# Kernel tuning notes

Measured on AMD Instinct MI355X. Metric: run time of the kernel, lower is better.

## Reference

```python
import jax, jax.numpy as jnp
import numpy as np

B, S = 4, 64
D, H, DFF, L, V = 512, 8, 2048, 2, 32128
DH = D // H
MAX_ITER, PAD_ID, TEMP = 16, 0, 1.0
NEG = -1e9


def rms_norm(x, w):
    # T5-style RMSNorm (no mean subtraction, no bias)
    return x * jax.lax.rsqrt(jnp.mean(x * x, axis=-1, keepdims=True) + 1e-6) * w


def mha(q_in, kv_in, wq, wk, wv, wo, bias):
    b, tq = q_in.shape[:2]
    tk = kv_in.shape[1]
    q = (q_in @ wq).reshape(b, tq, H, DH)
    k = (kv_in @ wk).reshape(b, tk, H, DH)
    v = (kv_in @ wv).reshape(b, tk, H, DH)
    scores = jnp.einsum('bqhd,bkhd->bhqk', q, k) * (1.0 / np.sqrt(DH)) + bias
    attn = jax.nn.softmax(scores, axis=-1)
    out = jnp.einsum('bhqk,bkhd->bqhd', attn, v).reshape(b, tq, D)
    return out @ wo


def setup_inputs() -> dict:
    key = jax.random.key(0)
    ks = iter(jax.random.split(key, 40))
    def w(*shape):
        return jax.random.normal(next(ks), shape, jnp.float32) * 0.02
    return {
        'input_ids': jax.random.randint(next(ks), (B, S), 0, V),
        'attention_mask': jnp.ones((B, S), jnp.float32),
        'emb': w(V, D),
        'enc_wq': w(L, D, D), 'enc_wk': w(L, D, D), 'enc_wv': w(L, D, D), 'enc_wo': w(L, D, D),
        'enc_ln1': jnp.ones((L, D), jnp.float32),
        'enc_w1': w(L, D, DFF), 'enc_w2': w(L, DFF, D),
        'enc_ln2': jnp.ones((L, D), jnp.float32),
        'enc_lnf': jnp.ones((D,), jnp.float32),
        'dec_sq': w(L, D, D), 'dec_sk': w(L, D, D), 'dec_sv': w(L, D, D), 'dec_so': w(L, D, D),
        'dec_ln1': jnp.ones((L, D), jnp.float32),
        'dec_cq': w(L, D, D), 'dec_ck': w(L, D, D), 'dec_cv': w(L, D, D), 'dec_co': w(L, D, D),
        'dec_ln2': jnp.ones((L, D), jnp.float32),
        'dec_w1': w(L, D, DFF), 'dec_w2': w(L, DFF, D),
        'dec_ln3': jnp.ones((L, D), jnp.float32),
        'dec_lnf': jnp.ones((D,), jnp.float32),
        'lm_head': w(D, V),
    }


def _encoder(x, bias, wq, wk, wv, wo, ln1, w1, w2, ln2, lnf):
    for l in range(L):
        h = rms_norm(x, ln1[l])
        x = x + mha(h, h, wq[l], wk[l], wv[l], wo[l], bias)
        h = rms_norm(x, ln2[l])
        x = x + jax.nn.relu(h @ w1[l]) @ w2[l]
    return rms_norm(x, lnf)


def _decoder(y, hs, enc_bias, sq, sk, sv, so, ln1, cq, ck, cv, co, ln2, w1, w2, ln3, lnf):
    t = y.shape[1]
    causal = jnp.where(jnp.tril(jnp.ones((t, t), bool)), 0.0, NEG)[None, None]  # [1,1,t,t]
    x = y
    for l in range(L):
        h = rms_norm(x, ln1[l])
        x = x + mha(h, h, sq[l], sk[l], sv[l], so[l], causal)
        h = rms_norm(x, ln2[l])
        x = x + mha(h, hs, cq[l], ck[l], cv[l], co[l], enc_bias)
        h = rms_norm(x, ln3[l])
        x = x + jax.nn.relu(h @ w1[l]) @ w2[l]
    return rms_norm(x, lnf)


def reference(input_ids, attention_mask, emb, enc_wq, enc_wk, enc_wv, enc_wo, enc_ln1, enc_w1, enc_w2, enc_ln2, enc_lnf, dec_sq, dec_sk, dec_sv, dec_so, dec_ln1, dec_cq, dec_ck, dec_cv, dec_co, dec_ln2, dec_w1, dec_w2, dec_ln3, dec_lnf, lm_head):
    enc_bias = (1.0 - attention_mask)[:, None, None, :] * NEG  # [B,1,1,S]
    hs = _encoder(emb[input_ids], enc_bias, enc_wq, enc_wk, enc_wv, enc_wo, enc_ln1, enc_w1, enc_w2, enc_ln2, enc_lnf)
    n = input_ids.shape[0]
    # decoder starts from the pad-token embedding, like T2A's pad_ids
    y = jnp.broadcast_to(emb[PAD_ID][None, None, :], (n, 1, D))
    probs_h, preds_h = [], []
    for _ in range(MAX_ITER):
        # full decoder re-run on the growing sequence: NO KV cache, as in the source
        dec_out = _decoder(y, hs, enc_bias, dec_sq, dec_sk, dec_sv, dec_so, dec_ln1, dec_cq, dec_ck, dec_cv, dec_co, dec_ln2, dec_w1, dec_w2, dec_ln3, dec_lnf)
        # grammar mask from NextTokens trackers is external state; treated as allow-all (zeros)
        logits = (dec_out[:, -1] @ lm_head) / TEMP  # [B,V]
        probs = jax.nn.softmax(logits, axis=-1)
        probs_h.append(probs)
        preds_h.append(jnp.argmax(probs, axis=-1))
        # differentiable soft embedding lookup: probs @ embedding matrix
        y = jnp.concatenate([y, (probs @ emb)[:, None, :]], axis=1)
    prob_history = jnp.stack(probs_h, axis=1)  # [B,T,V]
    pred_history = jnp.stack(preds_h, axis=1)  # [B,T]
    return prob_history, pred_history == PAD_ID
```

## Files before the change

kernel.cpp:

```cpp
#include <hip/hip_runtime.h>
#include <math.h>

#define BB   4
#define SS   64
#define DD   512
#define HH   8
#define DHH  64
#define DFFF 2048
#define LL   2
#define VV   32128
#define TT   16
#define EPSV 1e-6f
#define NEGB (-1e9f)
#define NTHR 256
#define NCH  502
#define STS  512

#define BSDc ((size_t)131072)
#define DD2c ((size_t)262144)


__global__ __launch_bounds__(NTHR) void k_embed(const int* __restrict__ ids,
        const float* __restrict__ emb, float* __restrict__ xe, float* __restrict__ xd,
        float* __restrict__ accb) {
    int blk = blockIdx.x, tid = threadIdx.x;
    int id = ids[blk];
    const float* src = emb + (size_t)id * DD;
    float* dst = xe + (size_t)blk * DD;
    for (int k = tid; k < DD; k += NTHR) dst[k] = src[k];
    if (blk < BB) {
        float* xdp = xd + (size_t)blk * DD;
        for (int k = tid; k < DD; k += NTHR) xdp[k] = emb[k];
    }
    if (blk == 4) {
        for (int k = tid; k < 2 * LL * 2048; k += NTHR) accb[k] = 0.f;
    }
}

__global__ __launch_bounds__(NTHR) void k_rms(const float* __restrict__ x,
        const float* __restrict__ ln, float* __restrict__ h) {
    __shared__ float sm[NTHR];
    int row = blockIdx.x, tid = threadIdx.x;
    const float* xr = x + (size_t)row * DD;
    float local = 0.f;
    for (int k = tid; k < DD; k += NTHR) { float v = xr[k]; local += v * v; }
    sm[tid] = local; __syncthreads();
    for (int s = 128; s > 0; s >>= 1) { if (tid < s) sm[tid] += sm[tid + s]; __syncthreads(); }
    float scale = 1.0f / sqrtf(sm[0] / DD + EPSV);
    for (int k = tid; k < DD; k += NTHR) h[(size_t)row * DD + k] = xr[k] * scale * ln[k];
}

__device__ __forceinline__ void gemm_part(const float* __restrict__ A,
        const float* __restrict__ W, float* __restrict__ P,
        int K, int N, int tile, int ks, int kcnt, float* sm) {
    float* As0 = sm;
    float* Ws0 = sm + 1040;
    float* As1 = sm + 2064;
    float* Ws1 = sm + 3104;
    const int tid = threadIdx.x, tr = tid >> 4, tc = tid & 15;
    const int nb = N >> 6;
    const int row0 = (tile / nb) * 64, col0 = (tile % nb) * 64;
    const int arow = tid >> 4, acol = tid & 15;
    const int wrow = tid >> 6, wcol = tid & 63;
    const int kb = ks * kcnt * 16;
    float av[4], wv[4];
    {
        int k0 = kb;
        #pragma unroll
        for (int j = 0; j < 4; j++) {
            av[j] = A[(size_t)(row0 + arow + j * 16) * K + k0 + acol];
            wv[j] = W[(size_t)(k0 + wrow + j * 4) * N + col0 + wcol];
        }
        #pragma unroll
        for (int j = 0; j < 4; j++) {
            As0[acol * 65 + arow + j * 16] = av[j];
            Ws0[(wrow + j * 4) * 64 + wcol] = wv[j];
        }
    }
    __syncthreads();
    float acc[4][4] = {};
    for (int s = 0; s < kcnt; s++) {
        float* Ac = (s & 1) ? As1 : As0;
        float* Wc = (s & 1) ? Ws1 : Ws0;
        if (s + 1 < kcnt) {
            int k0 = kb + (s + 1) * 16;
            #pragma unroll
            for (int j = 0; j < 4; j++) {
                av[j] = A[(size_t)(row0 + arow + j * 16) * K + k0 + acol];
                wv[j] = W[(size_t)(k0 + wrow + j * 4) * N + col0 + wcol];
            }
        }
        #pragma unroll
        for (int kk = 0; kk < 16; kk++) {
            float a[4], b[4];
            #pragma unroll
            for (int j = 0; j < 4; j++) { a[j] = Ac[kk * 65 + tr * 4 + j]; b[j] = Wc[kk * 64 + tc * 4 + j]; }
            #pragma unroll
            for (int r = 0; r < 4; r++)
                #pragma unroll
                for (int c = 0; c < 4; c++) acc[r][c] += a[r] * b[c];
        }
        __syncthreads();
        if (s + 1 < kcnt) {
            float* An = (s & 1) ? As0 : As1;
            float* Wn = (s & 1) ? Ws0 : Ws1;
            #pragma unroll
            for (int j = 0; j < 4; j++) {
                An[acol * 65 + arow + j * 16] = av[j];
                Wn[(wrow + j * 4) * 64 + wcol] = wv[j];
            }
            __syncthreads();
        }
    }
    #pragma unroll
    for (int r = 0; r < 4; r++)
        #pragma unroll
        for (int c = 0; c < 4; c++)
            P[(tr * 4 + r) * 64 + tc * 4 + c] = acc[r][c];
}

template<int KS, int KCNT>
__global__ __launch_bounds__(NTHR) void k_sk(const float* __restrict__ A,
        const float* __restrict__ W, float* __restrict__ P, int K, int N) {
    __shared__ float sm[4128];
    int tile = blockIdx.x / KS, ks = blockIdx.x % KS;
    gemm_part(A, W, P + (size_t)blockIdx.x * 4096, K, N, tile, ks, KCNT, sm);
}

template<int KS, int KCNT>
__global__ __launch_bounds__(NTHR) void k_qkvsk(const float* __restrict__ A,
        const float* __restrict__ wq, const float* __restrict__ wk, const float* __restrict__ wv,
        float* __restrict__ P) {
    __shared__ float sm[4128];
    int j = blockIdx.x / KS, ks = blockIdx.x % KS;
    int m = j >> 5, t2 = j & 31;
    const float* W = (m == 0) ? wq : (m == 1 ? wk : wv);
    gemm_part(A, W, P + (size_t)blockIdx.x * 4096, 512, 512, t2, ks, KCNT, sm);
}

template<int KS, int KCNT>
__global__ __launch_bounds__(NTHR) void k_ckcvsk(const float* __restrict__ A,
        const float* __restrict__ wck, const float* __restrict__ wcv, float* __restrict__ P) {
    __shared__ float sm[4128];
    int j = blockIdx.x / KS, ks = blockIdx.x % KS;
    int m = j >> 5, t2 = j & 31;
    const float* W = (m < 2) ? (wck + (size_t)m * DD2c) : (wcv + (size_t)(m - 2) * DD2c);
    gemm_part(A, W, P + (size_t)blockIdx.x * 4096, 512, 512, t2, ks, KCNT, sm);
}

__device__ __forceinline__ void red_part(const float* __restrict__ P, float* __restrict__ C,
        const float* __restrict__ res, int N, int relu, int tile, int sidx, int KS) {
    const int tid = threadIdx.x;
    const int nb = N >> 6;
    const int row0 = (tile / nb) * 64, col0 = (tile % nb) * 64;
    const float* Pb = P + (size_t)sidx * KS * 4096;
    for (int o = tid; o < 4096; o += NTHR) {
        float v = 0.f;
        for (int k = 0; k < KS; k++) v += Pb[(size_t)k * 4096 + o];
        int r = o >> 6, c = o & 63;
        size_t ix = (size_t)(row0 + r) * N + col0 + c;
        if (res) v += res[ix];
        if (relu) v = fmaxf(v, 0.f);
        C[ix] = v;
    }
}

template<int KS>
__global__ __launch_bounds__(NTHR) void k_red(const float* __restrict__ P, float* __restrict__ C,
        const float* __restrict__ res, int N, int relu) {
    red_part(P, C, res, N, relu, blockIdx.x, blockIdx.x, KS);
}

template<int KS>
__global__ __launch_bounds__(NTHR) void k_qkvred(const float* __restrict__ P, float* __restrict__ qkv) {
    int j = blockIdx.x, m = j >> 5, t2 = j & 31;
    red_part(P, qkv + (size_t)m * BSDc, nullptr, 512, 0, t2, j, KS);
}

template<int KS>
__global__ __launch_bounds__(NTHR) void k_ckcvred(const float* __restrict__ P,
        float* __restrict__ cK, float* __restrict__ cV) {
    int j = blockIdx.x, m = j >> 5, t2 = j & 31;
    float* C = (m < 2) ? (cK + (size_t)m * BSDc) : (cV + (size_t)(m - 2) * BSDc);
    red_part(P, C, nullptr, 512, 0, t2, j, KS);
}

__global__ __launch_bounds__(NTHR) void k_eattn(const float* __restrict__ qkv,
        const float* __restrict__ mask, float* __restrict__ o) {
    __shared__ float sm[3 * 64 * 65];
    int job = blockIdx.x;
    int b = job / HH, h = job % HH;
    int tid = threadIdx.x;
    int lane = tid & 63, wave = tid >> 6;
    float* qq = sm;
    float* kk = sm + 64 * 65;
    float* vv = sm + 2 * 64 * 65;
    for (int i = tid; i < SS * DHH; i += NTHR) {
        int s = i >> 6, d = i & 63;
        size_t src = (size_t)(b * SS + s) * DD + h * DHH + d;
        qq[s * 65 + d] = qkv[src];
        kk[s * 65 + d] = qkv[BSDc + src];
        vv[s * 65 + d] = qkv[2 * BSDc + src];
    }
    __syncthreads();
    float bias = (1.0f - mask[b * SS + lane]) * NEGB;
    for (int r = 0; r < 16; r++) {
        int s = wave * 16 + r;
        float sc = 0.f;
        for (int i = 0; i < DHH; i++) sc += qq[s * 65 + i] * kk[lane * 65 + i];
        sc = sc * 0.125f + bias;
        float m = sc;
        for (int o2 = 32; o2 > 0; o2 >>= 1) m = fmaxf(m, __shfl_xor(m, o2));
        float e = expf(sc - m);
        float sum = e;
        for (int o2 = 32; o2 > 0; o2 >>= 1) sum += __shfl_xor(sum, o2);
        float p = e / sum;
        float acc = 0.f;
        for (int t2 = 0; t2 < SS; t2++) acc += __shfl(p, t2) * vv[t2 * 65 + lane];
        o[(size_t)(b * SS + s) * DD + h * DHH + lane] = acc;
    }
}


__device__ __forceinline__ void build_hAT(const float* __restrict__ A, const float* __restrict__ a1,
        const float* __restrict__ a2, const float* __restrict__ ln, float* hAT, float* scl) {
    const int tid = threadIdx.x, lane = tid & 63, wv = tid >> 6;
    for (int k = tid; k < DD; k += NTHR) {
        float4 h;
        h.x = A[k]; h.y = A[DD + k]; h.z = A[2 * DD + k]; h.w = A[3 * DD + k];
        if (a1) { h.x += a1[k]; h.y += a1[DD + k]; h.z += a1[2 * DD + k]; h.w += a1[3 * DD + k]; }
        if (a2) { h.x += a2[k]; h.y += a2[DD + k]; h.z += a2[2 * DD + k]; h.w += a2[3 * DD + k]; }
        *(float4*)(hAT + (size_t)k * 4) = h;
    }
    __syncthreads();
    float loc = 0.f;
    for (int k = lane; k < DD; k += 64) { float x = hAT[k * 4 + wv]; loc += x * x; }
    for (int o = 32; o > 0; o >>= 1) loc += __shfl_xor(loc, o);
    if (lane == 0) scl[wv] = 1.0f / sqrtf(loc / DD + EPSV);
    __syncthreads();
    float s0 = scl[0], s1 = scl[1], s2 = scl[2], s3 = scl[3];
    for (int k = tid; k < DD; k += NTHR) {
        float lw = ln[k];
        float4 h = *(float4*)(hAT + (size_t)k * 4);
        h.x *= s0 * lw; h.y *= s1 * lw; h.z *= s2 * lw; h.w *= s3 * lw;
        *(float4*)(hAT + (size_t)k * 4) = h;
    }
    __syncthreads();
}

template<int K, int NC>
__device__ __forceinline__ void gemv_core(const float* hAT, const float* __restrict__ W,
        int N, int col0, float* red, float* outL) {
    constexpr int C4N = NC / 4;
    constexpr int KSN = NTHR / C4N;
    constexpr int KC  = K / KSN;
    const int tid = threadIdx.x;
    const int c4 = tid % C4N, ks = tid / C4N;
    const float4* W4 = (const float4*)W;
    float acc[4][4] = {};
    const int kb = ks * KC;
    #pragma unroll 8
    for (int kk = 0; kk < KC; kk++) {
        int k = kb + kk;
        float4 w4 = W4[(size_t)k * (N >> 2) + (col0 >> 2) + c4];
        float4 h4 = *(const float4*)(hAT + (size_t)k * 4);
        float hb[4] = {h4.x, h4.y, h4.z, h4.w};
        float wb[4] = {w4.x, w4.y, w4.z, w4.w};
        #pragma unroll
        for (int b = 0; b < 4; b++)
            #pragma unroll
            for (int ci = 0; ci < 4; ci++) acc[b][ci] += hb[b] * wb[ci];
    }
    {
        float* rp = red + (size_t)ks * (NC * 4) + c4 * 4;
        #pragma unroll
        for (int b = 0; b < 4; b++)
            #pragma unroll
            for (int ci = 0; ci < 4; ci++) rp[b * NC + ci] = acc[b][ci];
    }
    __syncthreads();
    for (int o = tid; o < 4 * NC; o += NTHR) {
        float v = 0.f;
        #pragma unroll
        for (int k2 = 0; k2 < KSN; k2++) v += red[(size_t)k2 * (NC * 4) + o];
        outL[o] = v;
    }
    __syncthreads();
}

__device__ __forceinline__ void oproj_add(const float* attT, const float* __restrict__ Wo,
        int h, float* accD, float* red) {
    const int tid = threadIdx.x;
    const int c4 = tid & 127, ks = tid >> 7;
    const float4* W4 = (const float4*)Wo;
    float ac[4][4] = {};
    const int db = ks * 32;
    #pragma unroll 8
    for (int dd = 0; dd < 32; dd++) {
        int d = db + dd;
        float4 w4 = W4[(size_t)(h * DHH + d) * 128 + c4];
        float wb[4] = {w4.x, w4.y, w4.z, w4.w};
        #pragma unroll
        for (int bb = 0; bb < 4; bb++) {
            float av = attT[d * 4 + bb];
            #pragma unroll
            for (int ci = 0; ci < 4; ci++) ac[bb][ci] += av * wb[ci];
        }
    }
    {
        float* rp = red + ks * 2048 + c4 * 4;
        #pragma unroll
        for (int bb = 0; bb < 4; bb++)
            #pragma unroll
            for (int ci = 0; ci < 4; ci++) rp[bb * 512 + ci] = ac[bb][ci];
    }
    __syncthreads();
    for (int o = tid; o < 2048; o += NTHR) {
        atomicAdd(accD + o, red[o] + red[2048 + o]);
    }
}

__global__ __launch_bounds__(NTHR) void k_self(const float* __restrict__ xc,
        const float* __restrict__ ln1, const float* __restrict__ Wq,
        const float* __restrict__ Wk, const float* __restrict__ Wv,
        const float* __restrict__ Wso, float* __restrict__ sKl, float* __restrict__ sVl,
        float* __restrict__ aS, int tt) {
    __shared__ float hAT[2048];
    __shared__ float red[4096];
    __shared__ float scl[4];
    __shared__ float qh[256];
    __shared__ float kh[256];
    __shared__ float vh[256];
    __shared__ float attT[256];
    const int h = blockIdx.x;
    const int tid = threadIdx.x, lane = tid & 63, b = tid >> 6;

    build_hAT(xc, nullptr, nullptr, ln1, hAT, scl);
    gemv_core<512, 64>(hAT, Wq, 512, h * 64, red, qh);
    gemv_core<512, 64>(hAT, Wk, 512, h * 64, red, kh);
    gemv_core<512, 64>(hAT, Wv, 512, h * 64, red, vh);
    {
        int c = tid & 63;
        size_t dst = ((size_t)b * TT + tt) * DD + h * DHH + c;
        sKl[dst] = kh[tid];
        sVl[dst] = vh[tid];
    }
    float sc = -1e30f;
    if (lane <= tt) {
        float s2 = 0.f;
        if (lane == tt) {
            #pragma unroll 16
            for (int i = 0; i < DHH; i++) s2 += qh[b * 64 + i] * kh[b * 64 + i];
        } else {
            const float* kr = sKl + ((size_t)b * TT + lane) * DD + h * DHH;
            #pragma unroll 16
            for (int i = 0; i < DHH; i++) s2 += qh[b * 64 + i] * kr[i];
        }
        sc = s2 * 0.125f;
    }
    float m = sc;
    for (int o2 = 32; o2 > 0; o2 >>= 1) m = fmaxf(m, __shfl_xor(m, o2));
    float e = (lane <= tt) ? expf(sc - m) : 0.f;
    float sum = e;
    for (int o2 = 32; o2 > 0; o2 >>= 1) sum += __shfl_xor(sum, o2);
    float pr = e / sum;
    float acc = 0.f;
    for (int j = 0; j < tt; j++) {
        float pj = __shfl(pr, j);
        acc += pj * sVl[((size_t)b * TT + j) * DD + h * DHH + lane];
    }
    acc += __shfl(pr, tt) * vh[b * 64 + lane];
    attT[lane * 4 + b] = acc;
    __syncthreads();
    oproj_add(attT, Wso, h, aS, red);
}

__global__ __launch_bounds__(NTHR) void k_cross(const float* __restrict__ xc,
        const float* __restrict__ aS, const float* __restrict__ ln2,
        const float* __restrict__ Wcq, const float* __restrict__ Wco,
        const float* __restrict__ cKl, const float* __restrict__ cVl,
        const float* __restrict__ mask, float* __restrict__ aC) {
    __shared__ float hAT[2048];
    __shared__ float red[4096];
    __shared__ float scl[4];
    __shared__ float qh[256];
    __shared__ float prS[256];
    __shared__ float attT[256];
    const int h = blockIdx.x;
    const int tid = threadIdx.x, lane = tid & 63, b = tid >> 6;

    build_hAT(xc, aS, nullptr, ln2, hAT, scl);
    gemv_core<512, 64>(hAT, Wcq, 512, h * 64, red, qh);
    const float* kr = cKl + ((size_t)b * SS + lane) * DD + h * DHH;
    float s2 = 0.f;
    #pragma unroll 16
    for (int i = 0; i < DHH; i++) s2 += qh[b * 64 + i] * kr[i];
    float sc = s2 * 0.125f + (1.0f - mask[b * SS + lane]) * NEGB;
    float m = sc;
    for (int o2 = 32; o2 > 0; o2 >>= 1) m = fmaxf(m, __shfl_xor(m, o2));
    float e = expf(sc - m);
    float sum = e;
    for (int o2 = 32; o2 > 0; o2 >>= 1) sum += __shfl_xor(sum, o2);
    prS[b * 64 + lane] = e / sum;
    const float* vbase = cVl + (size_t)b * SS * DD + h * DHH + lane;
    float a0 = 0.f, a1 = 0.f, a2 = 0.f, a3 = 0.f;
    #pragma unroll 4
    for (int j = 0; j < SS; j += 4) {
        a0 += prS[b * 64 + j]     * vbase[(size_t)j * DD];
        a1 += prS[b * 64 + j + 1] * vbase[(size_t)(j + 1) * DD];
        a2 += prS[b * 64 + j + 2] * vbase[(size_t)(j + 2) * DD];
        a3 += prS[b * 64 + j + 3] * vbase[(size_t)(j + 3) * DD];
    }
    attT[lane * 4 + b] = (a0 + a1) + (a2 + a3);
    __syncthreads();
    oproj_add(attT, Wco, h, aC, red);
}

template<int K, int NC>
__global__ __launch_bounds__(NTHR) void k_gemv(const float* __restrict__ A,
        const float* __restrict__ a1, const float* __restrict__ a2, const float* __restrict__ ln,
        const float* __restrict__ W, float* __restrict__ O, int ostr, int N,
        const float* __restrict__ res, const float* __restrict__ r1, const float* __restrict__ r2,
        int relu) {
    constexpr int C4N = NC / 4;
    constexpr int KSN = NTHR / C4N;
    constexpr int KC  = K / KSN;
    __shared__ float sm[K * 4 + 4096 + 4];
    float* hAT = sm;
    float* red = sm + K * 4;
    float* scl = sm + K * 4 + 4096;
    const int tid = threadIdx.x, lane = tid & 63, wv = tid >> 6;
    for (int k = tid; k < K; k += NTHR) {
        float4 h;
        h.x = A[k]; h.y = A[K + k]; h.z = A[2 * K + k]; h.w = A[3 * K + k];
        if (a1) { h.x += a1[k]; h.y += a1[K + k]; h.z += a1[2 * K + k]; h.w += a1[3 * K + k]; }
        if (a2) { h.x += a2[k]; h.y += a2[K + k]; h.z += a2[2 * K + k]; h.w += a2[3 * K + k]; }
        *(float4*)(hAT + (size_t)k * 4) = h;
    }
    __syncthreads();
    if (ln) {
        float loc = 0.f;
        for (int k = lane; k < K; k += 64) { float x = hAT[k * 4 + wv]; loc += x * x; }
        for (int o = 32; o > 0; o >>= 1) loc += __shfl_xor(loc, o);
        if (lane == 0) scl[wv] = 1.0f / sqrtf(loc / K + EPSV);
        __syncthreads();
        float s0 = scl[0], s1 = scl[1], s2 = scl[2], s3 = scl[3];
        for (int k = tid; k < K; k += NTHR) {
            float lw = ln[k];
            float4 h = *(float4*)(hAT + (size_t)k * 4);
            h.x *= s0 * lw; h.y *= s1 * lw; h.z *= s2 * lw; h.w *= s3 * lw;
            *(float4*)(hAT + (size_t)k * 4) = h;
        }
    }
    __syncthreads();
    const int c4 = tid % C4N, ks = tid / C4N;
    const float4* W4 = (const float4*)W;
    const int col0 = blockIdx.x * NC;
    float acc[4][4] = {};
    const int kb = ks * KC;
    #pragma unroll 8
    for (int kk = 0; kk < KC; kk++) {
        int k = kb + kk;
        float4 w4 = W4[(size_t)k * (N >> 2) + (col0 >> 2) + c4];
        float4 h4 = *(float4*)(hAT + (size_t)k * 4);
        float hb[4] = {h4.x, h4.y, h4.z, h4.w};
        float wb[4] = {w4.x, w4.y, w4.z, w4.w};
        #pragma unroll
        for (int b = 0; b < 4; b++)
            #pragma unroll
            for (int ci = 0; ci < 4; ci++) acc[b][ci] += hb[b] * wb[ci];
    }
    {
        float* rp = red + (size_t)ks * (NC * 4) + c4 * 4;
        #pragma unroll
        for (int b = 0; b < 4; b++)
            #pragma unroll
            for (int ci = 0; ci < 4; ci++) rp[b * NC + ci] = acc[b][ci];
    }
    __syncthreads();
    for (int o = tid; o < 4 * NC; o += NTHR) {
        int b = o / NC, c = o % NC;
        float v = 0.f;
        #pragma unroll
        for (int k2 = 0; k2 < KSN; k2++) v += red[(size_t)k2 * (NC * 4) + o];
        size_t ix = (size_t)b * ostr + col0 + c;
        if (res) v += res[ix];
        if (r1)  v += r1[ix];
        if (r2)  v += r2[ix];
        if (relu) v = fmaxf(v, 0.f);
        O[ix] = v;
    }
}

__global__ __launch_bounds__(NTHR) void k_lmhead(const float* __restrict__ xc, float* __restrict__ xn,
        const float* __restrict__ lnf, const float* __restrict__ Wlm,
        float* __restrict__ lgb, float* __restrict__ stm, float* __restrict__ sts,
        int* __restrict__ stix, float* __restrict__ accb) {
    int blk = blockIdx.x, tid = threadIdx.x, lane = tid & 63, wave = tid >> 6;
    if (blk >= NCH) {
        for (int k = tid; k < BB * DD; k += NTHR) xn[k] = 0.f;
        for (int k = tid; k < 2 * LL * 2048; k += NTHR) accb[k] = 0.f;
        return;
    }
    __shared__ float hAT[2048];
    __shared__ float red[4096];
    __shared__ float msc[4];
    __shared__ float lgl[256];
    for (int k = tid; k < DD; k += NTHR) {
        float4 r;
        r.x = xc[k];          r.y = xc[DD + k];
        r.z = xc[2 * DD + k]; r.w = xc[3 * DD + k];
        *(float4*)(hAT + (size_t)k * 4) = r;
    }
    __syncthreads();
    {
        float loc = 0.f;
        for (int k = lane; k < DD; k += 64) { float x = hAT[k * 4 + wave]; loc += x * x; }
        for (int o = 32; o > 0; o >>= 1) loc += __shfl_xor(loc, o);
        if (lane == 0) msc[wave] = 1.0f / sqrtf(loc / DD + EPSV);
    }
    __syncthreads();
    float s0 = msc[0], s1 = msc[1], s2 = msc[2], s3 = msc[3];
    for (int k = tid; k < DD; k += NTHR) {
        float lw = lnf[k];
        float4 r = *(float4*)(hAT + (size_t)k * 4);
        r.x *= s0 * lw; r.y *= s1 * lw; r.z *= s2 * lw; r.w *= s3 * lw;
        *(float4*)(hAT + (size_t)k * 4) = r;
    }
    __syncthreads();
    {
        int c4 = tid & 15, ks = tid >> 4;
        const float4* W4 = (const float4*)Wlm;
        float acc[4][4] = {};
        int kb = ks * 32;
        #pragma unroll
        for (int kk = 0; kk < 32; kk++) {
            int k = kb + kk;
            float4 w4 = W4[(size_t)k * (VV >> 2) + blk * 16 + c4];
            float4 h4 = *(float4*)(hAT + (size_t)k * 4);
            float hb[4] = {h4.x, h4.y, h4.z, h4.w};
            float wb[4] = {w4.x, w4.y, w4.z, w4.w};
            #pragma unroll
            for (int b = 0; b < 4; b++)
                #pragma unroll
                for (int ci = 0; ci < 4; ci++) acc[b][ci] += hb[b] * wb[ci];
        }
        float* rp = red + ks * 256 + c4 * 4;
        #pragma unroll
        for (int b = 0; b < 4; b++)
            #pragma unroll
            for (int ci = 0; ci < 4; ci++) rp[b * 64 + ci] = acc[b][ci];
    }
    __syncthreads();
    {
        float v = 0.f;
        #pragma unroll
        for (int k2 = 0; k2 < 16; k2++) v += red[k2 * 256 + tid];
        lgl[tid] = v;
        lgb[(size_t)(tid >> 6) * VV + blk * 64 + (tid & 63)] = v;
    }
    __syncthreads();
    {
        int b = wave;
        float v0 = lgl[b * 64 + lane];
        float mx = v0; int ix = lane;
        for (int o = 32; o > 0; o >>= 1) {
            float om = __shfl_xor(mx, o); int oi = __shfl_xor(ix, o);
            if (om > mx || (om == mx && oi < ix)) { mx = om; ix = oi; }
        }
        float s = expf(v0 - mx);
        for (int o = 32; o > 0; o >>= 1) s += __shfl_xor(s, o);
        if (lane == 0) {
            stm[b * STS + blk] = mx;
            sts[b * STS + blk] = s;
            stix[b * STS + blk] = blk * 64 + ix;
        }
    }
}

__global__ __launch_bounds__(NTHR) void k_dmerge(const float* __restrict__ lgb,
        const float* __restrict__ stm, const float* __restrict__ sts, const int* __restrict__ stix,
        const float* __restrict__ emb, float* __restrict__ out, float* __restrict__ xn, int tt) {
    __shared__ float mM[8];
    __shared__ int jS[4];
    __shared__ float pT[256];
    __shared__ float red[4096];
    int blk = blockIdx.x, tid = threadIdx.x, lane = tid & 63, wave = tid >> 6;
    {
        int b = wave;
        float M = -1e30f, S = 0.f; int jb = 0;
        for (int j = lane; j < NCH; j += 64) {
            float mj = stm[b * STS + j], sj = sts[b * STS + j];
            if (mj > M) { S = S * expf(M - mj) + sj; M = mj; jb = j; }
            else        { S += sj * expf(mj - M); }
        }
        for (int o = 32; o > 0; o >>= 1) {
            float Mo = __shfl_xor(M, o), So = __shfl_xor(S, o);
            int jo = __shfl_xor(jb, o);
            if (Mo > M || (Mo == M && jo < jb)) { S = S * expf(M - Mo) + So; M = Mo; jb = jo; }
            else { S += So * expf(Mo - M); }
        }
        if (lane == 0) { mM[b] = M; mM[4 + b] = S; jS[b] = jb; }
    }
    __syncthreads();
    if (blk < NCH) {
        {
            int b = tid >> 6, c = tid & 63;
            float lg = lgb[(size_t)b * VV + blk * 64 + c];
            float p = expf(lg - mM[b]) / mM[4 + b];
            out[((size_t)b * TT + tt) * VV + blk * 64 + c] = p;
            pT[c * 4 + b] = p;
        }
        __syncthreads();
        {
            int c4 = tid & 127, rs = tid >> 7;
            const float4* E4 = (const float4*)emb;
            float4 a0 = {0,0,0,0}, a1 = a0, a2 = a0, a3 = a0;
            int rb = rs * 32;
            #pragma unroll 8
            for (int r = 0; r < 32; r++) {
                int row = rb + r;
                float4 e4 = E4[((size_t)(blk * 64 + row)) * 128 + c4];
                float4 p4 = *(float4*)(pT + row * 4);
                a0.x += p4.x * e4.x; a0.y += p4.x * e4.y; a0.z += p4.x * e4.z; a0.w += p4.x * e4.w;
                a1.x += p4.y * e4.x; a1.y += p4.y * e4.y; a1.z += p4.y * e4.z; a1.w += p4.y * e4.w;
                a2.x += p4.z * e4.x; a2.y += p4.z * e4.y; a2.z += p4.z * e4.z; a2.w += p4.z * e4.w;
                a3.x += p4.w * e4.x; a3.y += p4.w * e4.y; a3.z += p4.w * e4.z; a3.w += p4.w * e4.w;
            }
            float* rp = red + rs * 2048 + c4 * 4;
            rp[0]        = a0.x; rp[1]        = a0.y; rp[2]        = a0.z; rp[3]        = a0.w;
            rp[512 + 0]  = a1.x; rp[512 + 1]  = a1.y; rp[512 + 2]  = a1.z; rp[512 + 3]  = a1.w;
            rp[1024 + 0] = a2.x; rp[1024 + 1] = a2.y; rp[1024 + 2] = a2.z; rp[1024 + 3] = a2.w;
            rp[1536 + 0] = a3.x; rp[1536 + 1] = a3.y; rp[1536 + 2] = a3.z; rp[1536 + 3] = a3.w;
        }
        __syncthreads();
        #pragma unroll
        for (int i = 0; i < 8; i++) {
            int o = tid + i * 256;
            atomicAdd(xn + o, red[o] + red[2048 + o]);
        }
    } else {
        if (tid < 4) {
            int col = stix[tid * STS + jS[tid]];
            out[(size_t)BB * TT * VV + tid * TT + tt] = (col == 0) ? 1.0f : 0.0f;
        }
    }
}

extern "C" void kernel_launch(void* const* d_in, const int* in_sizes, int n_in,
                              void* d_out, int out_size, void* d_ws, size_t ws_size,
                              hipStream_t stream) {
    const int*   ids     = (const int*)  d_in[0];
    const float* mask    = (const float*)d_in[1];
    const float* emb     = (const float*)d_in[2];
    const float* enc_wq  = (const float*)d_in[3];
    const float* enc_wk  = (const float*)d_in[4];
    const float* enc_wv  = (const float*)d_in[5];
    const float* enc_wo  = (const float*)d_in[6];
    const float* enc_ln1 = (const float*)d_in[7];
    const float* enc_w1  = (const float*)d_in[8];
    const float* enc_w2  = (const float*)d_in[9];
    const float* enc_ln2 = (const float*)d_in[10];
    const float* enc_lnf = (const float*)d_in[11];
    const float* dec_sq  = (const float*)d_in[12];
    const float* dec_sk  = (const float*)d_in[13];
    const float* dec_sv  = (const float*)d_in[14];
    const float* dec_so  = (const float*)d_in[15];
    const float* dec_ln1 = (const float*)d_in[16];
    const float* dec_cq  = (const float*)d_in[17];
    const float* dec_ck  = (const float*)d_in[18];
    const float* dec_cv  = (const float*)d_in[19];
    const float* dec_co  = (const float*)d_in[20];
    const float* dec_ln2 = (const float*)d_in[21];
    const float* dec_w1  = (const float*)d_in[22];
    const float* dec_w2  = (const float*)d_in[23];
    const float* dec_ln3 = (const float*)d_in[24];
    const float* dec_lnf = (const float*)d_in[25];
    const float* lm_head = (const float*)d_in[26];
    float* out = (float*)d_out;

    float* ws    = (float*)d_ws;
    float* xe    = ws;
    float* qkv   = xe + BSDc;
    float* hbuf  = qkv + 3 * BSDc;
    float* attb  = hbuf + BSDc;
    float* ffbuf = attb + BSDc;
    float* cK    = ffbuf + (size_t)BB * SS * DFFF;
    float* cV    = cK + LL * BSDc;
    float* sK    = cV + LL * BSDc;
    float* sV    = sK + (size_t)LL * BB * TT * DD;
    float* xdA   = sV + (size_t)LL * BB * TT * DD;
    float* xdB   = xdA + 2048;
    float* accb  = xdB + 2048;
    float* dff   = accb + 8192;
    float* stm   = dff + 8192;
    float* sts   = stm + 4 * STS;
    int*   stix  = (int*)(sts + 4 * STS);
    float* lgb   = (float*)(stix) + 2048;
    float* skb   = lgb + 4 * VV;

    k_embed<<<256, NTHR, 0, stream>>>(ids, emb, xe, xdA, accb);
    for (int l = 0; l < LL; l++) {
        k_rms<<<256, NTHR, 0, stream>>>(xe, enc_ln1 + (size_t)l * DD, hbuf);
        k_qkvsk<4, 8><<<384, NTHR, 0, stream>>>(hbuf, enc_wq + (size_t)l * DD2c,
                enc_wk + (size_t)l * DD2c, enc_wv + (size_t)l * DD2c, skb);
        k_qkvred<4><<<96, NTHR, 0, stream>>>(skb, qkv);
        k_eattn<<<32, NTHR, 0, stream>>>(qkv, mask, attb);
        k_sk<8, 4><<<256, NTHR, 0, stream>>>(attb, enc_wo + (size_t)l * DD2c, skb, 512, 512);
        k_red<8><<<32, NTHR, 0, stream>>>(skb, xe, xe, 512, 0);
        k_rms<<<256, NTHR, 0, stream>>>(xe, enc_ln2 + (size_t)l * DD, hbuf);
        k_sk<4, 8><<<512, NTHR, 0, stream>>>(hbuf, enc_w1 + (size_t)l * DD * DFFF, skb, 512, 2048);
        k_red<4><<<128, NTHR, 0, stream>>>(skb, ffbuf, nullptr, 2048, 1);
        k_sk<16, 8><<<512, NTHR, 0, stream>>>(ffbuf, enc_w2 + (size_t)l * DFFF * DD, skb, 2048, 512);
        k_red<16><<<32, NTHR, 0, stream>>>(skb, xe, xe, 512, 0);
    }
    k_rms<<<256, NTHR, 0, stream>>>(xe, enc_lnf, hbuf);
    k_ckcvsk<4, 8><<<512, NTHR, 0, stream>>>(hbuf, dec_ck, dec_cv, skb);
    k_ckcvred<4><<<128, NTHR, 0, stream>>>(skb, cK, cV);

    for (int tt = 0; tt < TT; tt++) {
        float* xc = (tt & 1) ? xdB : xdA;
        float* xn = (tt & 1) ? xdA : xdB;
        for (int l = 0; l < LL; l++) {
            float* aS = accb + (size_t)l * 2048;
            float* aC = accb + 4096 + (size_t)l * 2048;
            k_self<<<HH, NTHR, 0, stream>>>(xc, dec_ln1 + (size_t)l * DD,
                    dec_sq + (size_t)l * DD2c, dec_sk + (size_t)l * DD2c,
                    dec_sv + (size_t)l * DD2c, dec_so + (size_t)l * DD2c,
                    sK + (size_t)l * BB * TT * DD, sV + (size_t)l * BB * TT * DD, aS, tt);
            k_cross<<<HH, NTHR, 0, stream>>>(xc, aS, dec_ln2 + (size_t)l * DD,
                    dec_cq + (size_t)l * DD2c, dec_co + (size_t)l * DD2c,
                    cK + (size_t)l * BSDc, cV + (size_t)l * BSDc, mask, aC);
            k_gemv<512, 16><<<128, NTHR, 0, stream>>>(xc, aS, aC, dec_ln3 + (size_t)l * DD,
                    dec_w1 + (size_t)l * DD * DFFF, dff, DFFF, DFFF,
                    nullptr, nullptr, nullptr, 1);
            k_gemv<2048, 8><<<64, NTHR, 0, stream>>>(dff, nullptr, nullptr, nullptr,
                    dec_w2 + (size_t)l * DFFF * DD, xc, DD, 512,
                    xc, aS, aC, 0);
        }
        k_lmhead<<<NCH + 1, NTHR, 0, stream>>>(xc, xn, dec_lnf, lm_head, lgb, stm, sts, stix, accb);
        k_dmerge<<<NCH + 1, NTHR, 0, stream>>>(lgb, stm, sts, stix, emb, out, xn, tt);
    }
}
```

Before: 2.533 ms.

## Fuse decoder FFN up/down into one kernel with atomic residual accumulators

```diff
diff --git a/kernel.cpp b/kernel.cpp
--- a/kernel.cpp
+++ b/kernel.cpp
@@ -15,6 +15,7 @@
 #define NTHR 256
 #define NCH  502
 #define STS  512
+#define NACCT (3 * LL)
 
 #define BSDc ((size_t)131072)
 #define DD2c ((size_t)262144)
@@ -33,7 +34,7 @@
         for (int k = tid; k < DD; k += NTHR) xdp[k] = emb[k];
     }
     if (blk == 4) {
-        for (int k = tid; k < 2 * LL * 2048; k += NTHR) accb[k] = 0.f;
+        for (int k = tid; k < NACCT * 2048; k += NTHR) accb[k] = 0.f;
     }
 }
 
@@ -222,14 +223,17 @@
 }
 
 
-__device__ __forceinline__ void build_hAT(const float* __restrict__ A, const float* __restrict__ a1,
-        const float* __restrict__ a2, const float* __restrict__ ln, float* hAT, float* scl) {
+__device__ __forceinline__ void build_hAT_n(const float* __restrict__ x0,
+        const float* __restrict__ accb, int nacc,
+        const float* __restrict__ ln, float* hAT, float* scl) {
     const int tid = threadIdx.x, lane = tid & 63, wv = tid >> 6;
     for (int k = tid; k < DD; k += NTHR) {
         float4 h;
-        h.x = A[k]; h.y = A[DD + k]; h.z = A[2 * DD + k]; h.w = A[3 * DD + k];
-        if (a1) { h.x += a1[k]; h.y += a1[DD + k]; h.z += a1[2 * DD + k]; h.w += a1[3 * DD + k]; }
-        if (a2) { h.x += a2[k]; h.y += a2[DD + k]; h.z += a2[2 * DD + k]; h.w += a2[3 * DD + k]; }
+        h.x = x0[k]; h.y = x0[DD + k]; h.z = x0[2 * DD + k]; h.w = x0[3 * DD + k];
+        for (int a = 0; a < nacc; a++) {
+            const float* ap = accb + (size_t)a * 2048;
+            h.x += ap[k]; h.y += ap[DD + k]; h.z += ap[2 * DD + k]; h.w += ap[3 * DD + k];
+        }
         *(float4*)(hAT + (size_t)k * 4) = h;
     }
     __syncthreads();
@@ -321,10 +325,11 @@
 }
 
 __global__ __launch_bounds__(NTHR) void k_self(const float* __restrict__ xc,
+        const float* __restrict__ accb, float* __restrict__ accw, int nacc,
         const float* __restrict__ ln1, const float* __restrict__ Wq,
         const float* __restrict__ Wk, const float* __restrict__ Wv,
         const float* __restrict__ Wso, float* __restrict__ sKl, float* __restrict__ sVl,
-        float* __restrict__ aS, int tt) {
+        int tt) {
     __shared__ float hAT[2048];
     __shared__ float red[4096];
     __shared__ float scl[4];
@@ -334,8 +339,9 @@
     __shared__ float attT[256];
     const int h = blockIdx.x;
     const int tid = threadIdx.x, lane = tid & 63, b = tid >> 6;
-
-    build_hAT(xc, nullptr, nullptr, ln1, hAT, scl);
+    float* aS = accw + (size_t)nacc * 2048;
+
+    build_hAT_n(xc, accb, nacc, ln1, hAT, scl);
     gemv_core<512, 64>(hAT, Wq, 512, h * 64, red, qh);
     gemv_core<512, 64>(hAT, Wk, 512, h * 64, red, kh);
     gemv_core<512, 64>(hAT, Wv, 512, h * 64, red, vh);
@@ -376,10 +382,10 @@
 }
 
 __global__ __launch_bounds__(NTHR) void k_cross(const float* __restrict__ xc,
-        const float* __restrict__ aS, const float* __restrict__ ln2,
-        const float* __restrict__ Wcq, const float* __restrict__ Wco,
-        const float* __restrict__ cKl, const float* __restrict__ cVl,
-        const float* __restrict__ mask, float* __restrict__ aC) {
+        const float* __restrict__ accb, float* __restrict__ accw, int nacc,
+        const float* __restrict__ ln2, const float* __restrict__ Wcq,
+        const float* __restrict__ Wco, const float* __restrict__ cKl,
+        const float* __restrict__ cVl, const float* __restrict__ mask) {
     __shared__ float hAT[2048];
     __shared__ float red[4096];
     __shared__ float scl[4];
@@ -388,8 +394,9 @@
     __shared__ float attT[256];
     const int h = blockIdx.x;
     const int tid = threadIdx.x, lane = tid & 63, b = tid >> 6;
-
-    build_hAT(xc, aS, nullptr, ln2, hAT, scl);
+    float* aC = accw + (size_t)nacc * 2048;
+
+    build_hAT_n(xc, accb, nacc, ln2, hAT, scl);
     gemv_core<512, 64>(hAT, Wcq, 512, h * 64, red, qh);
     const float* kr = cKl + ((size_t)b * SS + lane) * DD + h * DHH;
     float s2 = 0.f;
@@ -416,118 +423,66 @@
     oproj_add(attT, Wco, h, aC, red);
 }
 
-template<int K, int NC>
-__global__ __launch_bounds__(NTHR) void k_gemv(const float* __restrict__ A,
-        const float* __restrict__ a1, const float* __restrict__ a2, const float* __restrict__ ln,
-        const float* __restrict__ W, float* __restrict__ O, int ostr, int N,
-        const float* __restrict__ res, const float* __restrict__ r1, const float* __restrict__ r2,
-        int relu) {
-    constexpr int C4N = NC / 4;
-    constexpr int KSN = NTHR / C4N;
-    constexpr int KC  = K / KSN;
-    __shared__ float sm[K * 4 + 4096 + 4];
-    float* hAT = sm;
-    float* red = sm + K * 4;
-    float* scl = sm + K * 4 + 4096;
-    const int tid = threadIdx.x, lane = tid & 63, wv = tid >> 6;
-    for (int k = tid; k < K; k += NTHR) {
-        float4 h;
-        h.x = A[k]; h.y = A[K + k]; h.z = A[2 * K + k]; h.w = A[3 * K + k];
-        if (a1) { h.x += a1[k]; h.y += a1[K + k]; h.z += a1[2 * K + k]; h.w += a1[3 * K + k]; }
-        if (a2) { h.x += a2[k]; h.y += a2[K + k]; h.z += a2[2 * K + k]; h.w += a2[3 * K + k]; }
-        *(float4*)(hAT + (size_t)k * 4) = h;
-    }
-    __syncthreads();
-    if (ln) {
-        float loc = 0.f;
-        for (int k = lane; k < K; k += 64) { float x = hAT[k * 4 + wv]; loc += x * x; }
-        for (int o = 32; o > 0; o >>= 1) loc += __shfl_xor(loc, o);
-        if (lane == 0) scl[wv] = 1.0f / sqrtf(loc / K + EPSV);
-        __syncthreads();
-        float s0 = scl[0], s1 = scl[1], s2 = scl[2], s3 = scl[3];
-        for (int k = tid; k < K; k += NTHR) {
-            float lw = ln[k];
-            float4 h = *(float4*)(hAT + (size_t)k * 4);
-            h.x *= s0 * lw; h.y *= s1 * lw; h.z *= s2 * lw; h.w *= s3 * lw;
-            *(float4*)(hAT + (size_t)k * 4) = h;
-        }
-    }
-    __syncthreads();
-    const int c4 = tid % C4N, ks = tid / C4N;
-    const float4* W4 = (const float4*)W;
-    const int col0 = blockIdx.x * NC;
-    float acc[4][4] = {};
-    const int kb = ks * KC;
-    #pragma unroll 8
-    for (int kk = 0; kk < KC; kk++) {
-        int k = kb + kk;
-        float4 w4 = W4[(size_t)k * (N >> 2) + (col0 >> 2) + c4];
-        float4 h4 = *(float4*)(hAT + (size_t)k * 4);
-        float hb[4] = {h4.x, h4.y, h4.z, h4.w};
-        float wb[4] = {w4.x, w4.y, w4.z, w4.w};
-        #pragma unroll
-        for (int b = 0; b < 4; b++)
-            #pragma unroll
-            for (int ci = 0; ci < 4; ci++) acc[b][ci] += hb[b] * wb[ci];
-    }
-    {
-        float* rp = red + (size_t)ks * (NC * 4) + c4 * 4;
-        #pragma unroll
-        for (int b = 0; b < 4; b++)
-            #pragma unroll
-            for (int ci = 0; ci < 4; ci++) rp[b * NC + ci] = acc[b][ci];
-    }
-    __syncthreads();
-    for (int o = tid; o < 4 * NC; o += NTHR) {
-        int b = o / NC, c = o % NC;
-        float v = 0.f;
-        #pragma unroll
-        for (int k2 = 0; k2 < KSN; k2++) v += red[(size_t)k2 * (NC * 4) + o];
-        size_t ix = (size_t)b * ostr + col0 + c;
-        if (res) v += res[ix];
-        if (r1)  v += r1[ix];
-        if (r2)  v += r2[ix];
-        if (relu) v = fmaxf(v, 0.f);
-        O[ix] = v;
+__global__ __launch_bounds__(NTHR) void k_ffn(const float* __restrict__ xc,
+        const float* __restrict__ accb, float* __restrict__ accw, int nacc,
+        const float* __restrict__ ln3, const float* __restrict__ W1,
+        const float* __restrict__ W2) {
+    __shared__ float hAT[2048];
+    __shared__ float red[4096];
+    __shared__ float scl[4];
+    __shared__ float upL[64];
+    const int j = blockIdx.x;
+    const int tid = threadIdx.x;
+    float* aF = accw + (size_t)nacc * 2048;
+
+    build_hAT_n(xc, accb, nacc, ln3, hAT, scl);
+    gemv_core<512, 16>(hAT, W1, DFFF, j * 16, red, upL);
+    {
+        const int c4 = tid & 127, ks = tid >> 7;
+        const float4* W24 = (const float4*)W2;
+        float ac[4][4] = {};
+        const int kb = ks * 8;
+        #pragma unroll
+        for (int kk = 0; kk < 8; kk++) {
+            int row = j * 16 + kb + kk;
+            float4 w4 = W24[(size_t)row * 128 + c4];
+            float wb[4] = {w4.x, w4.y, w4.z, w4.w};
+            #pragma unroll
+            for (int bb = 0; bb < 4; bb++) {
+                float av = fmaxf(upL[bb * 16 + kb + kk], 0.f);
+                #pragma unroll
+                for (int ci = 0; ci < 4; ci++) ac[bb][ci] += av * wb[ci];
+            }
+        }
+        float* rp = red + ks * 2048 + c4 * 4;
+        #pragma unroll
+        for (int bb = 0; bb < 4; bb++)
+            #pragma unroll
+            for (int ci = 0; ci < 4; ci++) rp[bb * 512 + ci] = ac[bb][ci];
+    }
+    __syncthreads();
+    for (int o0 = tid; o0 < 2048; o0 += NTHR) {
+        int bb = o0 >> 9, n = (o0 + j * 16) & 511;
+        int o = bb * 512 + n;
+        atomicAdd(aF + o, red[o] + red[2048 + o]);
     }
 }
 
 __global__ __launch_bounds__(NTHR) void k_lmhead(const float* __restrict__ xc, float* __restrict__ xn,
-        const float* __restrict__ lnf, const float* __restrict__ Wlm,
-        float* __restrict__ lgb, float* __restrict__ stm, float* __restrict__ sts,
-        int* __restrict__ stix, float* __restrict__ accb) {
+        const float* __restrict__ accb, const float* __restrict__ lnf,
+        const float* __restrict__ Wlm, float* __restrict__ lgb, float* __restrict__ stm,
+        float* __restrict__ sts, int* __restrict__ stix, float* __restrict__ accz) {
     int blk = blockIdx.x, tid = threadIdx.x, lane = tid & 63, wave = tid >> 6;
     if (blk >= NCH) {
         for (int k = tid; k < BB * DD; k += NTHR) xn[k] = 0.f;
-        for (int k = tid; k < 2 * LL * 2048; k += NTHR) accb[k] = 0.f;
+        for (int k = tid; k < NACCT * 2048; k += NTHR) accz[k] = 0.f;
         return;
     }
     __shared__ float hAT[2048];
     __shared__ float red[4096];
     __shared__ float msc[4];
     __shared__ float lgl[256];
-    for (int k = tid; k < DD; k += NTHR) {
-        float4 r;
-        r.x = xc[k];          r.y = xc[DD + k];
-        r.z = xc[2 * DD + k]; r.w = xc[3 * DD + k];
-        *(float4*)(hAT + (size_t)k * 4) = r;
-    }
-    __syncthreads();
-    {
-        float loc = 0.f;
-        for (int k = lane; k < DD; k += 64) { float x = hAT[k * 4 + wave]; loc += x * x; }
-        for (int o = 32; o > 0; o >>= 1) loc += __shfl_xor(loc, o);
-        if (lane == 0) msc[wave] = 1.0f / sqrtf(loc / DD + EPSV);
-    }
-    __syncthreads();
-    float s0 = msc[0], s1 = msc[1], s2 = msc[2], s3 = msc[3];
-    for (int k = tid; k < DD; k += NTHR) {
-        float lw = lnf[k];
-        float4 r = *(float4*)(hAT + (size_t)k * 4);
-        r.x *= s0 * lw; r.y *= s1 * lw; r.z *= s2 * lw; r.w *= s3 * lw;
-        *(float4*)(hAT + (size_t)k * 4) = r;
-    }
-    __syncthreads();
+    build_hAT_n(xc, accb, NACCT, lnf, hAT, msc);
     {
         int c4 = tid & 15, ks = tid >> 4;
         const float4* W4 = (const float4*)Wlm;
@@ -692,8 +647,7 @@
     float* xdA   = sV + (size_t)LL * BB * TT * DD;
     float* xdB   = xdA + 2048;
     float* accb  = xdB + 2048;
-    float* dff   = accb + 8192;
-    float* stm   = dff + 8192;
+    float* stm   = accb + NACCT * 2048;
     float* sts   = stm + 4 * STS;
     int*   stix  = (int*)(sts + 4 * STS);
     float* lgb   = (float*)(stix) + 2048;
@@ -722,23 +676,21 @@
         float* xc = (tt & 1) ? xdB : xdA;
         float* xn = (tt & 1) ? xdA : xdB;
         for (int l = 0; l < LL; l++) {
-            float* aS = accb + (size_t)l * 2048;
-            float* aC = accb + 4096 + (size_t)l * 2048;
-            k_self<<<HH, NTHR, 0, stream>>>(xc, dec_ln1 + (size_t)l * DD,
+            k_self<<<HH, NTHR, 0, stream>>>(xc, accb, accb, 3 * l,
+                    dec_ln1 + (size_t)l * DD,
                     dec_sq + (size_t)l * DD2c, dec_sk + (size_t)l * DD2c,
                     dec_sv + (size_t)l * DD2c, dec_so + (size_t)l * DD2c,
-                    sK + (size_t)l * BB * TT * DD, sV + (size_t)l * BB * TT * DD, aS, tt);
-            k_cross<<<HH, NTHR, 0, stream>>>(xc, aS, dec_ln2 + (size_t)l * DD,
+                    sK + (size_t)l * BB * TT * DD, sV + (size_t)l * BB * TT * DD, tt);
+            k_cross<<<HH, NTHR, 0, stream>>>(xc, accb, accb, 3 * l + 1,
+                    dec_ln2 + (size_t)l * DD,
                     dec_cq + (size_t)l * DD2c, dec_co + (size_t)l * DD2c,
-                    cK + (size_t)l * BSDc, cV + (size_t)l * BSDc, mask, aC);
-            k_gemv<512, 16><<<128, NTHR, 0, stream>>>(xc, aS, aC, dec_ln3 + (size_t)l * DD,
-                    dec_w1 + (size_t)l * DD * DFFF, dff, DFFF, DFFF,
-                    nullptr, nullptr, nullptr, 1);
-            k_gemv<2048, 8><<<64, NTHR, 0, stream>>>(dff, nullptr, nullptr, nullptr,
-                    dec_w2 + (size_t)l * DFFF * DD, xc, DD, 512,
-                    xc, aS, aC, 0);
-        }
-        k_lmhead<<<NCH + 1, NTHR, 0, stream>>>(xc, xn, dec_lnf, lm_head, lgb, stm, sts, stix, accb);
+                    cK + (size_t)l * BSDc, cV + (size_t)l * BSDc, mask);
+            k_ffn<<<128, NTHR, 0, stream>>>(xc, accb, accb, 3 * l + 2,
+                    dec_ln3 + (size_t)l * DD,
+                    dec_w1 + (size_t)l * DD * DFFF, dec_w2 + (size_t)l * DFFF * DD);
+        }
+        k_lmhead<<<NCH + 1, NTHR, 0, stream>>>(xc, xn, accb, dec_lnf, lm_head,
+                lgb, stm, sts, stix, accb);
         k_dmerge<<<NCH + 1, NTHR, 0, stream>>>(lgb, stm, sts, stix, emb, out, xn, tt);
     }
 }
```

Result: faster. 2.367 ms (-6.6%).
